# Kernel optimization log

Measured on AMD Instinct MI355X. Metric: run time of the kernel, lower is better.

## Reference

```python
import jax, jax.numpy as jnp
import numpy as np

RADIUS = 5
REG_TH = 10.0
BIG_KEY = 2**30


def setup_inputs() -> dict:
    key = jax.random.key(0)
    k1, k2, k3, k4 = jax.random.split(key, 4)
    B, L, A, R = 32, 6, 1024, 1024
    pre_hough = jax.random.normal(k1, (B, 1, A, R), dtype=jnp.float32)
    gt_hough = jax.random.uniform(k2, (B, 1, A, R), dtype=jnp.float32)
    in_pre_points = jax.random.randint(k3, (B, L, 2), 0, 1000, dtype=jnp.int32)
    gt_points = jax.random.randint(k4, (B, L, 2), 0, 1000, dtype=jnp.int32)
    return {"pre_hough": pre_hough, "gt_hough": gt_hough,
            "in_pre_points": in_pre_points, "gt_points": gt_points}


def reference(pre_hough, gt_hough, in_pre_points, gt_points):
    B, _, A, R = pre_hough.shape  # A = Angle (height), R = Rho (width)
    L = gt_points.shape[1]
    ph = jax.nn.sigmoid(pre_hough)

    # sort pre points per batch by x*10000 + y; invalid (x<0) points sort last (padding)
    px, py = in_pre_points[..., 0], in_pre_points[..., 1]
    sort_key = jnp.where(px < 0, BIG_KEY, px * 10000 + py)
    order = jnp.argsort(sort_key, axis=1)
    pre_pts = jnp.take_along_axis(in_pre_points, order[..., None], axis=1)  # [B,L,2]

    use_gt = gt_points[..., 0] >= 0
    pt = jnp.where(use_gt[..., None], gt_points, pre_pts)  # [B,L,2]
    x, y = pt[..., 0], pt[..., 1]

    offs = jnp.arange(-RADIUS, RADIUS + 1)  # 11 offsets
    xi = x[..., None] + offs  # [B,L,11] indexes Angle axis
    yi = y[..., None] + offs  # [B,L,11] indexes Rho axis
    # original bounds x by width (Rho) and y by height (Angle); here A==R so consistent
    mx = (xi >= 0) & (xi < R)
    my = (yi >= 0) & (yi < A)
    xic = jnp.clip(xi, 0, A - 1)
    yic = jnp.clip(yi, 0, R - 1)

    b = jnp.arange(B)[:, None, None, None]
    pp = ph[b, 0, xic[:, :, :, None], yic[:, :, None, :]]        # [B,L,11,11]
    gp = gt_hough[b, 0, xic[:, :, :, None], yic[:, :, None, :]]  # [B,L,11,11]
    mask = (mx[:, :, :, None] & my[:, :, None, :]).astype(ph.dtype)

    per_pt = jnp.sum(jnp.abs(pp - gp) * mask, axis=(2, 3))  # [B,L]
    one_invalid = (pre_pts[..., 0] < 0) | (gt_points[..., 0] < 0)
    both_invalid = (pre_pts[..., 0] < 0) & (gt_points[..., 0] < 0)
    per_pt = per_pt * jnp.where(one_invalid, REG_TH, 1.0) / (RADIUS * RADIUS)
    per_pt = jnp.where(both_invalid, 0.0, per_pt)

    total = jnp.sum(per_pt)
    fallback = jnp.mean(jnp.abs(ph - gt_hough))  # F.l1_loss mean when no valid points
    return jnp.where(total == 0.0, fallback, total / B)
```

## Files before the change

kernel.cpp:

```cpp
#include <hip/hip_runtime.h>

#define RADIUS 5
#define DIAM 11
#define PATCH (DIAM * DIAM)
#define B_ 32
#define L_ 6
#define A_ 1024
#define R_ 1024
#define BIG_KEY (1 << 30)
#define REG_TH 10.0f
#define NPTS (B_ * L_)

__global__ void k_points(const float* __restrict__ pre, const float* __restrict__ gt,
                         const int* __restrict__ pre_pts, const int* __restrict__ gt_pts,
                         float* __restrict__ ws) {
    const int bl = blockIdx.x;
    const int b = bl / L_;
    const int l = bl % L_;

    __shared__ int sx, sy;
    __shared__ float sscale;

    if (threadIdx.x == 0) {
        int px[L_], py[L_];
        long long key[L_];
        for (int i = 0; i < L_; ++i) {
            px[i] = pre_pts[(b * L_ + i) * 2 + 0];
            py[i] = pre_pts[(b * L_ + i) * 2 + 1];
            key[i] = (px[i] < 0) ? (long long)BIG_KEY
                                 : (long long)px[i] * 10000 + (long long)py[i];
        }
        int o = 0;
        for (int i = 0; i < L_; ++i) {
            int r = 0;
            for (int j = 0; j < L_; ++j)
                if (key[j] < key[i] || (key[j] == key[i] && j < i)) ++r;
            if (r == l) { o = i; break; }
        }
        const int gx = gt_pts[(b * L_ + l) * 2 + 0];
        const int gy = gt_pts[(b * L_ + l) * 2 + 1];
        const int prx = px[o], pry = py[o];
        const bool use_gt = (gx >= 0);
        sx = use_gt ? gx : prx;
        sy = use_gt ? gy : pry;
        const bool one_inv = (prx < 0) || (gx < 0);
        const bool both_inv = (prx < 0) && (gx < 0);
        sscale = both_inv ? 0.0f
                          : (one_inv ? REG_TH : 1.0f) * (1.0f / (float)(RADIUS * RADIUS));
    }
    __syncthreads();

    const int t = threadIdx.x;
    float v = 0.0f;
    if (t < PATCH) {
        const int i = t / DIAM;
        const int j = t % DIAM;
        const int xi = sx - RADIUS + i;
        const int yi = sy - RADIUS + j;
        const bool m = (xi >= 0) && (xi < R_) && (yi >= 0) && (yi < A_);
        const int xic = min(max(xi, 0), A_ - 1);
        const int yic = min(max(yi, 0), R_ - 1);
        const size_t idx = (size_t)b * (size_t)(A_ * R_) + (size_t)xic * R_ + (size_t)yic;
        const float p = 1.0f / (1.0f + expf(-pre[idx]));
        const float g = gt[idx];
        v = m ? fabsf(p - g) : 0.0f;
    }

    for (int off = 32; off > 0; off >>= 1) v += __shfl_down(v, off, 64);
    __shared__ float partial[2];
    if ((t & 63) == 0) partial[t >> 6] = v;
    __syncthreads();
    if (t == 0) ws[bl] = (partial[0] + partial[1]) * sscale;
}

__global__ void k_finish(const float* __restrict__ pre, const float* __restrict__ gt,
                         const float* __restrict__ ws, float* __restrict__ out) {
    const int t = threadIdx.x;
    __shared__ float part[4];
    __shared__ float s_total;

    float v = (t < NPTS) ? ws[t] : 0.0f;
    for (int off = 32; off > 0; off >>= 1) v += __shfl_down(v, off, 64);
    if ((t & 63) == 0) part[t >> 6] = v;
    __syncthreads();
    if (t == 0) s_total = part[0] + part[1] + part[2] + part[3];
    __syncthreads();
    const float total = s_total;

    if (total != 0.0f) {
        if (t == 0) out[0] = total / (float)B_;
        return;
    }

    const size_t N = (size_t)B_ * (size_t)(A_ * R_);
    float acc = 0.0f;
    for (size_t i = t; i < N; i += (size_t)blockDim.x) {
        const float p = 1.0f / (1.0f + expf(-pre[i]));
        acc += fabsf(p - gt[i]);
    }
    for (int off = 32; off > 0; off >>= 1) acc += __shfl_down(acc, off, 64);
    if ((t & 63) == 0) part[t >> 6] = acc;
    __syncthreads();
    if (t == 0) out[0] = (part[0] + part[1] + part[2] + part[3]) / (float)N;
}

extern "C" void kernel_launch(void* const* d_in, const int* in_sizes, int n_in,
                              void* d_out, int out_size, void* d_ws, size_t ws_size,
                              hipStream_t stream) {
    const float* pre = (const float*)d_in[0];
    const float* gt = (const float*)d_in[1];
    const int* prep = (const int*)d_in[2];
    const int* gtp = (const int*)d_in[3];
    float* out = (float*)d_out;
    float* ws = (float*)d_ws;

    k_points<<<NPTS, 128, 0, stream>>>(pre, gt, prep, gtp, ws);
    k_finish<<<1, 256, 0, stream>>>(pre, gt, ws, out);
}
```

Before: 214.5 us.

## Fuse point and finish kernels via last-block atomic counter

Merges the per-point patch kernel and the final reduction kernel into one launch. A wrapping atomicInc counter stored in the workspace picks the last block to finish, and that block reduces the per-point sums and, if needed, runs the fallback full-tensor mean. This removes one kernel launch and the gap between the two kernels. The trade-off is that it relies on the counter starting at zero in the workspace and on atomicInc wrapping it back to zero for the next call. If the fallback path ever runs, it does so in a single 128-thread block instead of 256 threads.

```diff
diff --git a/kernel.cpp b/kernel.cpp
--- a/kernel.cpp
+++ b/kernel.cpp
@@ -11,17 +11,21 @@
 #define REG_TH 10.0f
 #define NPTS (B_ * L_)
 
-__global__ void k_points(const float* __restrict__ pre, const float* __restrict__ gt,
-                         const int* __restrict__ pre_pts, const int* __restrict__ gt_pts,
-                         float* __restrict__ ws) {
+__global__ void k_fused(const float* __restrict__ pre, const float* __restrict__ gt,
+                        const int* __restrict__ pre_pts, const int* __restrict__ gt_pts,
+                        float* __restrict__ ws, float* __restrict__ out) {
     const int bl = blockIdx.x;
     const int b = bl / L_;
     const int l = bl % L_;
+    const int t = threadIdx.x;
 
     __shared__ int sx, sy;
     __shared__ float sscale;
+    __shared__ float partial[2];
+    __shared__ int s_is_last;
+    __shared__ float s_total;
 
-    if (threadIdx.x == 0) {
+    if (t == 0) {
         int px[L_], py[L_];
         long long key[L_];
         for (int i = 0; i < L_; ++i) {
@@ -50,7 +54,6 @@
     }
     __syncthreads();
 
-    const int t = threadIdx.x;
     float v = 0.0f;
     if (t < PATCH) {
         const int i = t / DIAM;
@@ -67,23 +70,24 @@
     }
 
     for (int off = 32; off > 0; off >>= 1) v += __shfl_down(v, off, 64);
-    __shared__ float partial[2];
     if ((t & 63) == 0) partial[t >> 6] = v;
     __syncthreads();
-    if (t == 0) ws[bl] = (partial[0] + partial[1]) * sscale;
-}
 
-__global__ void k_finish(const float* __restrict__ pre, const float* __restrict__ gt,
-                         const float* __restrict__ ws, float* __restrict__ out) {
-    const int t = threadIdx.x;
-    __shared__ float part[4];
-    __shared__ float s_total;
+    if (t == 0) {
+        ws[bl] = (partial[0] + partial[1]) * sscale;
+        __threadfence();
+        unsigned int old = atomicInc((unsigned int*)(ws + NPTS), NPTS - 1u);
+        s_is_last = (old == NPTS - 2u);
+    }
+    __syncthreads();
+    if (!s_is_last) return;
 
-    float v = (t < NPTS) ? ws[t] : 0.0f;
-    for (int off = 32; off > 0; off >>= 1) v += __shfl_down(v, off, 64);
-    if ((t & 63) == 0) part[t >> 6] = v;
+    __threadfence();
+    float r = ws[t] + ((t < NPTS - 128) ? ws[t + 128] : 0.0f);
+    for (int off = 32; off > 0; off >>= 1) r += __shfl_down(r, off, 64);
+    if ((t & 63) == 0) partial[t >> 6] = r;
     __syncthreads();
-    if (t == 0) s_total = part[0] + part[1] + part[2] + part[3];
+    if (t == 0) s_total = partial[0] + partial[1];
     __syncthreads();
     const float total = s_total;
 
@@ -99,9 +103,9 @@
         acc += fabsf(p - gt[i]);
     }
     for (int off = 32; off > 0; off >>= 1) acc += __shfl_down(acc, off, 64);
-    if ((t & 63) == 0) part[t >> 6] = acc;
+    if ((t & 63) == 0) partial[t >> 6] = acc;
     __syncthreads();
-    if (t == 0) out[0] = (part[0] + part[1] + part[2] + part[3]) / (float)N;
+    if (t == 0) out[0] = (partial[0] + partial[1]) / (float)N;
 }
 
 extern "C" void kernel_launch(void* const* d_in, const int* in_sizes, int n_in,
@@ -114,6 +118,5 @@
     float* out = (float*)d_out;
     float* ws = (float*)d_ws;
 
-    k_points<<<NPTS, 128, 0, stream>>>(pre, gt, prep, gtp, ws);
-    k_finish<<<1, 256, 0, stream>>>(pre, gt, ws, out);
+    k_fused<<<NPTS, 128, 0, stream>>>(pre, gt, prep, gtp, ws, out);
 }
```

New measurement: 215.7 us. About the same (+0.6%).
